# Optimization experiments

Measured on AMD Instinct MI355X. Metric: run time of the kernel, lower is better.

The kernel has to match this reference:

```python
import jax, jax.numpy as jnp
import numpy as np


def setup_inputs() -> dict:
    key = jax.random.key(0)
    kq, kk, kv = jax.random.split(key, 3)
    B, H, S, D = 2, 16, 2048, 64
    Q = jax.random.normal(kq, (B, H, S, D), dtype=jnp.float32)
    K = jax.random.normal(kk, (B, H, S, D), dtype=jnp.float32)
    V = jax.random.normal(kv, (B, H, S, D), dtype=jnp.float32)
    return {"Q": Q, "K": K, "V": V}


def reference(Q, K, V):
    # Faithful to the torch module: NO 1/sqrt(d_k) scaling (d_k is computed
    # but never used in the original forward).
    scores = jnp.einsum('bhqd,bhkd->bhqk', Q, K)      # [B,H,S,S]
    attn = jax.nn.softmax(scores, axis=-1)
    out = jnp.einsum('bhqk,bhkd->bhqd', attn, V)      # [B,H,S,D]
    return out
```

## Files before the change

kernel.cpp:

```cpp
#include <hip/hip_runtime.h>


typedef __bf16 bf16_t;
typedef __bf16 bf16x8 __attribute__((ext_vector_type(8)));
typedef float  f32x16 __attribute__((ext_vector_type(16)));

constexpr int S  = 2048;
constexpr int Dh = 64;
constexpr int QT = 128;
constexpr int KT = 64;

__device__ __forceinline__ int sw(int row, int col) {
    return row * 64 + ((((col >> 3) ^ (row & 7)) << 3) | (col & 7));
}

__global__ __launch_bounds__(256)
void attn_mfma_kernel(const float* __restrict__ Qg,
                      const float* __restrict__ Kg,
                      const float* __restrict__ Vg,
                      float* __restrict__ Og)
{
    __shared__ bf16_t Khs[KT * Dh];
    __shared__ bf16_t Kls[KT * Dh];
    __shared__ bf16_t Vts[Dh * KT];
    __shared__ bf16_t Pbs[QT * Dh];

    const int tid  = threadIdx.x;
    const int lane = tid & 63;
    const int wv   = tid >> 6;
    const int l31  = lane & 31;
    const int l5   = lane >> 5;
    const int mbase = wv * 32;

    const int head = blockIdx.x >> 4;
    const int qt   = blockIdx.x & 15;

    const float* Qp = Qg + ((size_t)head * S + (size_t)qt * QT) * Dh;
    const float* Kp = Kg + (size_t)head * S * Dh;
    const float* Vp = Vg + (size_t)head * S * Dh;
    float*       Op = Og + ((size_t)head * S + (size_t)qt * QT) * Dh;

    bf16x8 qh[4], ql[4];
    {
        const float* qrow = Qp + (size_t)(mbase + l31) * Dh;
        #pragma unroll
        for (int ks = 0; ks < 4; ++ks) {
            const float* p = qrow + ks * 16 + l5 * 8;
            const float4 a = *(const float4*)(p);
            const float4 b = *(const float4*)(p + 4);
            const float xs[8] = {a.x, a.y, a.z, a.w, b.x, b.y, b.z, b.w};
            #pragma unroll
            for (int j = 0; j < 8; ++j) {
                const bf16_t h = (bf16_t)xs[j];
                qh[ks][j] = h;
                ql[ks][j] = (bf16_t)(xs[j] - (float)h);
            }
        }
    }

    f32x16 o0, o1;
    float  lp[16];
    #pragma unroll
    for (int r = 0; r < 16; ++r) { o0[r] = 0.f; o1[r] = 0.f; lp[r] = 0.f; }

    #pragma unroll 1
    for (int ch = 0; ch < S / KT; ++ch) {
        __syncthreads();

        {
            const float* Kc = Kp + (size_t)ch * KT * Dh;
            #pragma unroll
            for (int it = 0; it < 4; ++it) {
                const int f   = it * 256 + tid;
                const int key = f >> 4;
                const int c4  = (f & 15) * 4;
                const float4 kx = *(const float4*)(Kc + key * Dh + c4);
                const float xs[4] = {kx.x, kx.y, kx.z, kx.w};
                union { bf16_t h[4]; uint2 u; } ph, pl;
                #pragma unroll
                for (int j = 0; j < 4; ++j) {
                    const bf16_t h = (bf16_t)xs[j];
                    ph.h[j] = h;
                    pl.h[j] = (bf16_t)(xs[j] - (float)h);
                }
                const int off = sw(key, c4);
                *(uint2*)&Khs[off] = ph.u;
                *(uint2*)&Kls[off] = pl.u;
            }
            const float* Vc = Vp + (size_t)ch * KT * Dh;
            const int kb = (tid >> 4) * 4;
            const int c4 = (tid & 15) * 4;
            const float4 v0 = *(const float4*)(Vc + (size_t)(kb + 0) * Dh + c4);
            const float4 v1 = *(const float4*)(Vc + (size_t)(kb + 1) * Dh + c4);
            const float4 v2 = *(const float4*)(Vc + (size_t)(kb + 2) * Dh + c4);
            const float4 v3 = *(const float4*)(Vc + (size_t)(kb + 3) * Dh + c4);
            const float rs[4][4] = {{v0.x, v1.x, v2.x, v3.x},
                                    {v0.y, v1.y, v2.y, v3.y},
                                    {v0.z, v1.z, v2.z, v3.z},
                                    {v0.w, v1.w, v2.w, v3.w}};
            #pragma unroll
            for (int i = 0; i < 4; ++i) {
                union { bf16_t h[4]; uint2 u; } pv;
                #pragma unroll
                for (int j = 0; j < 4; ++j) pv.h[j] = (bf16_t)rs[i][j];
                *(uint2*)&Vts[sw(c4 + i, kb)] = pv.u;
            }
        }
        __syncthreads();

        f32x16 acc0, acc1;
        #pragma unroll
        for (int r = 0; r < 16; ++r) { acc0[r] = 0.f; acc1[r] = 0.f; }
        #pragma unroll
        for (int ks = 0; ks < 4; ++ks) {
            const int co = ks * 16 + l5 * 8;
            const bf16x8 bh0 = *(const bf16x8*)&Khs[sw(l31,      co)];
            const bf16x8 bh1 = *(const bf16x8*)&Khs[sw(32 + l31, co)];
            const bf16x8 bl0 = *(const bf16x8*)&Kls[sw(l31,      co)];
            const bf16x8 bl1 = *(const bf16x8*)&Kls[sw(32 + l31, co)];
            acc0 = __builtin_amdgcn_mfma_f32_32x32x16_bf16(qh[ks], bh0, acc0, 0, 0, 0);
            acc1 = __builtin_amdgcn_mfma_f32_32x32x16_bf16(qh[ks], bh1, acc1, 0, 0, 0);
            acc0 = __builtin_amdgcn_mfma_f32_32x32x16_bf16(qh[ks], bl0, acc0, 0, 0, 0);
            acc1 = __builtin_amdgcn_mfma_f32_32x32x16_bf16(qh[ks], bl1, acc1, 0, 0, 0);
            acc0 = __builtin_amdgcn_mfma_f32_32x32x16_bf16(ql[ks], bh0, acc0, 0, 0, 0);
            acc1 = __builtin_amdgcn_mfma_f32_32x32x16_bf16(ql[ks], bh1, acc1, 0, 0, 0);
        }

        #pragma unroll
        for (int r = 0; r < 16; ++r) {
            const int row = mbase + (r & 3) + 8 * (r >> 2) + 4 * l5;
            const float p0 = __expf(acc0[r]);
            const float p1 = __expf(acc1[r]);
            const bf16_t b0 = (bf16_t)p0;
            const bf16_t b1 = (bf16_t)p1;
            lp[r] += (float)b0 + (float)b1;
            Pbs[sw(row, l31)]      = b0;
            Pbs[sw(row, 32 + l31)] = b1;
        }

        #pragma unroll
        for (int ks = 0; ks < 4; ++ks) {
            const int co = ks * 16 + l5 * 8;
            const bf16x8 pa  = *(const bf16x8*)&Pbs[sw(mbase + l31, co)];
            const bf16x8 vb0 = *(const bf16x8*)&Vts[sw(l31,      co)];
            const bf16x8 vb1 = *(const bf16x8*)&Vts[sw(32 + l31, co)];
            o0 = __builtin_amdgcn_mfma_f32_32x32x16_bf16(pa, vb0, o0, 0, 0, 0);
            o1 = __builtin_amdgcn_mfma_f32_32x32x16_bf16(pa, vb1, o1, 0, 0, 0);
        }
    }

    #pragma unroll
    for (int r = 0; r < 16; ++r) {
        float v = lp[r];
        #pragma unroll
        for (int m = 1; m <= 16; m <<= 1) v += __shfl_xor(v, m, 64);
        lp[r] = v;
    }

    #pragma unroll
    for (int r = 0; r < 16; ++r) {
        const int row = mbase + (r & 3) + 8 * (r >> 2) + 4 * l5;
        const float inv = 1.0f / lp[r];
        Op[(size_t)row * Dh + l31]      = o0[r] * inv;
        Op[(size_t)row * Dh + 32 + l31] = o1[r] * inv;
    }
}

extern "C" void kernel_launch(void* const* d_in, const int* in_sizes, int n_in,
                              void* d_out, int out_size, void* d_ws, size_t ws_size,
                              hipStream_t stream)
{
    const float* Q = (const float*)d_in[0];
    const float* K = (const float*)d_in[1];
    const float* V = (const float*)d_in[2];
    float*       O = (float*)d_out;

    dim3 grid(32 * (S / QT));
    dim3 block(256);
    attn_mfma_kernel<<<grid, block, 0, stream>>>(Q, K, V, O);
}
```

Before: 169.9 us.

## Split key range across two blocks and combine partial results in second kernel

Each query tile now runs as two blocks that each process half of the key chunks. They write unnormalized partial outputs and row sums to workspace, and a separate combine kernel adds the halves and normalizes. The grid grows from 512 to 1024 blocks so the GPU's CUs are better occupied, and launch bounds now request 4 blocks per SM. The cost is an extra kernel launch plus a round trip of partial outputs through global memory. The split path runs only when the workspace is large enough, otherwise the old path is used.

Result: slower. 439.4 us (+158.6%).

```diff
diff --git a/kernel.cpp b/kernel.cpp
--- a/kernel.cpp
+++ b/kernel.cpp
@@ -14,11 +14,14 @@
     return row * 64 + ((((col >> 3) ^ (row & 7)) << 3) | (col & 7));
 }
 
-__global__ __launch_bounds__(256)
+template<bool SPLIT>
+__global__ __launch_bounds__(256, 4)
 void attn_mfma_kernel(const float* __restrict__ Qg,
                       const float* __restrict__ Kg,
                       const float* __restrict__ Vg,
-                      float* __restrict__ Og)
+                      float* __restrict__ Og,
+                      float* __restrict__ Opart,
+                      float* __restrict__ lpart)
 {
     __shared__ bf16_t Khs[KT * Dh];
     __shared__ bf16_t Kls[KT * Dh];
@@ -32,13 +35,16 @@
     const int l5   = lane >> 5;
     const int mbase = wv * 32;
 
-    const int head = blockIdx.x >> 4;
-    const int qt   = blockIdx.x & 15;
+    const int bx   = blockIdx.x;
+    const int head = SPLIT ? (bx >> 5) : (bx >> 4);
+    const int qt   = SPLIT ? ((bx >> 1) & 15) : (bx & 15);
+    const int half = SPLIT ? (bx & 1) : 0;
+    const int ch0  = SPLIT ? half * (S / KT / 2) : 0;
+    const int nch  = SPLIT ? (S / KT / 2) : (S / KT);
 
     const float* Qp = Qg + ((size_t)head * S + (size_t)qt * QT) * Dh;
     const float* Kp = Kg + (size_t)head * S * Dh;
     const float* Vp = Vg + (size_t)head * S * Dh;
-    float*       Op = Og + ((size_t)head * S + (size_t)qt * QT) * Dh;
 
     bf16x8 qh[4], ql[4];
     {
@@ -64,7 +70,8 @@
     for (int r = 0; r < 16; ++r) { o0[r] = 0.f; o1[r] = 0.f; lp[r] = 0.f; }
 
     #pragma unroll 1
-    for (int ch = 0; ch < S / KT; ++ch) {
+    for (int ci = 0; ci < nch; ++ci) {
+        const int ch = ch0 + ci;
         __syncthreads();
 
         {
@@ -157,13 +164,46 @@
         lp[r] = v;
     }
 
-    #pragma unroll
-    for (int r = 0; r < 16; ++r) {
-        const int row = mbase + (r & 3) + 8 * (r >> 2) + 4 * l5;
-        const float inv = 1.0f / lp[r];
-        Op[(size_t)row * Dh + l31]      = o0[r] * inv;
-        Op[(size_t)row * Dh + 32 + l31] = o1[r] * inv;
-    }
+    if (SPLIT) {
+        float* Po = Opart + (size_t)bx * (QT * Dh);
+        #pragma unroll
+        for (int r = 0; r < 16; ++r) {
+            const int row = mbase + (r & 3) + 8 * (r >> 2) + 4 * l5;
+            Po[(size_t)row * Dh + l31]      = o0[r];
+            Po[(size_t)row * Dh + 32 + l31] = o1[r];
+            if (l31 == 0) lpart[(size_t)bx * QT + row] = lp[r];
+        }
+    } else {
+        float* Op = Og + ((size_t)head * S + (size_t)qt * QT) * Dh;
+        #pragma unroll
+        for (int r = 0; r < 16; ++r) {
+            const int row = mbase + (r & 3) + 8 * (r >> 2) + 4 * l5;
+            const float inv = 1.0f / lp[r];
+            Op[(size_t)row * Dh + l31]      = o0[r] * inv;
+            Op[(size_t)row * Dh + 32 + l31] = o1[r] * inv;
+        }
+    }
+}
+
+__global__ __launch_bounds__(256)
+void combine_kernel(const float* __restrict__ Opart,
+                    const float* __restrict__ lpart,
+                    float* __restrict__ Og)
+{
+    const int i  = blockIdx.x * 256 + threadIdx.x;
+    const int q  = i >> 11;
+    const int rw = (i >> 4) & 127;
+    const size_t e = (size_t)(i & 2047) * 4;
+    const float4 a = *(const float4*)(Opart + (size_t)(2 * q)     * (QT * Dh) + e);
+    const float4 b = *(const float4*)(Opart + (size_t)(2 * q + 1) * (QT * Dh) + e);
+    const float  l = lpart[(size_t)(2 * q) * QT + rw] + lpart[(size_t)(2 * q + 1) * QT + rw];
+    const float inv = 1.0f / l;
+    float4 o;
+    o.x = (a.x + b.x) * inv;
+    o.y = (a.y + b.y) * inv;
+    o.z = (a.z + b.z) * inv;
+    o.w = (a.w + b.w) * inv;
+    *(float4*)(Og + (size_t)i * 4) = o;
 }
 
 extern "C" void kernel_launch(void* const* d_in, const int* in_sizes, int n_in,
@@ -175,7 +215,20 @@
     const float* V = (const float*)d_in[2];
     float*       O = (float*)d_out;
 
-    dim3 grid(32 * (S / QT));
-    dim3 block(256);
-    attn_mfma_kernel<<<grid, block, 0, stream>>>(Q, K, V, O);
-}
+    constexpr size_t NPART       = 1024;
+    constexpr size_t OPART_ELEMS = NPART * QT * Dh;
+    constexpr size_t LPART_ELEMS = NPART * QT;
+    constexpr size_t NEED = (OPART_ELEMS + LPART_ELEMS) * sizeof(float);
+
+    if (ws_size >= NEED) {
+        float* Opart = (float*)d_ws;
+        float* lpart = Opart + OPART_ELEMS;
+        attn_mfma_kernel<true><<<dim3(1024), dim3(256), 0, stream>>>(
+            Q, K, V, nullptr, Opart, lpart);
+        const int n4 = (int)(OPART_ELEMS / 2 / 4);
+        combine_kernel<<<dim3(n4 / 256), dim3(256), 0, stream>>>(Opart, lpart, O);
+    } else {
+        attn_mfma_kernel<false><<<dim3(512), dim3(256), 0, stream>>>(
+            Q, K, V, O, nullptr, nullptr);
+    }
+}
```

## Use single fp16 MFMA for QK^T with 16x16 tiles and 64-row query blocks

Applied to the files above, without the earlier changes.

Replaces the three-pass bf16 hi/lo split for Q·K^T with one fp16 MFMA per tile, which removes the low-part K buffer and roughly two thirds of the score MFMAs. Work moves from 32x32x16 to 16x16x32 MFMA shapes and each block now handles 64 query rows, doubling the grid, with a launch-bounds occupancy hint added. In exchange, every K/V chunk is loaded and converted twice as often across the grid, and fp16 scores carry less mantissa than the split bf16 scheme; softmax still runs without max subtraction.

Measured after the change: 189.5 us. 1.12x slower.

```diff
diff --git a/kernel.cpp b/kernel.cpp
--- a/kernel.cpp
+++ b/kernel.cpp
@@ -1,67 +1,66 @@
 #include <hip/hip_runtime.h>
 
 
-typedef __bf16 bf16_t;
-typedef __bf16 bf16x8 __attribute__((ext_vector_type(8)));
-typedef float  f32x16 __attribute__((ext_vector_type(16)));
+typedef __bf16    bf16_t;
+typedef _Float16  f16_t;
+typedef __bf16    bf16x8 __attribute__((ext_vector_type(8)));
+typedef _Float16  f16x8  __attribute__((ext_vector_type(8)));
+typedef float     f32x4  __attribute__((ext_vector_type(4)));
 
 constexpr int S  = 2048;
 constexpr int Dh = 64;
-constexpr int QT = 128;
 constexpr int KT = 64;
 
 __device__ __forceinline__ int sw(int row, int col) {
     return row * 64 + ((((col >> 3) ^ (row & 7)) << 3) | (col & 7));
 }
 
-__global__ __launch_bounds__(256)
-void attn_mfma_kernel(const float* __restrict__ Qg,
-                      const float* __restrict__ Kg,
-                      const float* __restrict__ Vg,
-                      float* __restrict__ Og)
+__global__ __launch_bounds__(256, 4)
+void attn_kernel(const float* __restrict__ Qg,
+                 const float* __restrict__ Kg,
+                 const float* __restrict__ Vg,
+                 float* __restrict__ Og)
 {
-    __shared__ bf16_t Khs[KT * Dh];
-    __shared__ bf16_t Kls[KT * Dh];
+    __shared__ f16_t  Khs[KT * Dh];
     __shared__ bf16_t Vts[Dh * KT];
-    __shared__ bf16_t Pbs[QT * Dh];
+    __shared__ bf16_t Pbs[64 * KT];
 
     const int tid  = threadIdx.x;
     const int lane = tid & 63;
     const int wv   = tid >> 6;
-    const int l31  = lane & 31;
-    const int l5   = lane >> 5;
-    const int mbase = wv * 32;
+    const int l15  = lane & 15;
+    const int qd   = lane >> 4;
+    const int wb   = wv * 16;
 
-    const int head = blockIdx.x >> 4;
-    const int qt   = blockIdx.x & 15;
+    const int head = blockIdx.x >> 5;
+    const int qt   = blockIdx.x & 31;
 
-    const float* Qp = Qg + ((size_t)head * S + (size_t)qt * QT) * Dh;
+    const float* Qp = Qg + ((size_t)head * S + (size_t)qt * 64) * Dh;
     const float* Kp = Kg + (size_t)head * S * Dh;
     const float* Vp = Vg + (size_t)head * S * Dh;
-    float*       Op = Og + ((size_t)head * S + (size_t)qt * QT) * Dh;
+    float*       Op = Og + ((size_t)head * S + (size_t)qt * 64) * Dh;
 
-    bf16x8 qh[4], ql[4];
+    f16x8 qf[2];
     {
-        const float* qrow = Qp + (size_t)(mbase + l31) * Dh;
+        const float* qrow = Qp + (size_t)(wb + l15) * Dh;
         #pragma unroll
-        for (int ks = 0; ks < 4; ++ks) {
-            const float* p = qrow + ks * 16 + l5 * 8;
+        for (int ks = 0; ks < 2; ++ks) {
+            const float* p = qrow + ks * 32 + qd * 8;
             const float4 a = *(const float4*)(p);
             const float4 b = *(const float4*)(p + 4);
             const float xs[8] = {a.x, a.y, a.z, a.w, b.x, b.y, b.z, b.w};
             #pragma unroll
-            for (int j = 0; j < 8; ++j) {
-                const bf16_t h = (bf16_t)xs[j];
-                qh[ks][j] = h;
-                ql[ks][j] = (bf16_t)(xs[j] - (float)h);
-            }
+            for (int j = 0; j < 8; ++j) qf[ks][j] = (f16_t)xs[j];
         }
     }
 
-    f32x16 o0, o1;
-    float  lp[16];
+    f32x4 oa[4];
+    float lp[4];
     #pragma unroll
-    for (int r = 0; r < 16; ++r) { o0[r] = 0.f; o1[r] = 0.f; lp[r] = 0.f; }
+    for (int t = 0; t < 4; ++t) {
+        oa[t] = (f32x4){0.f, 0.f, 0.f, 0.f};
+        lp[t] = 0.f;
+    }
 
     #pragma unroll 1
     for (int ch = 0; ch < S / KT; ++ch) {
@@ -76,16 +75,10 @@
                 const int c4  = (f & 15) * 4;
                 const float4 kx = *(const float4*)(Kc + key * Dh + c4);
                 const float xs[4] = {kx.x, kx.y, kx.z, kx.w};
-                union { bf16_t h[4]; uint2 u; } ph, pl;
+                union { f16_t h[4]; uint2 u; } ph;
                 #pragma unroll
-                for (int j = 0; j < 4; ++j) {
-                    const bf16_t h = (bf16_t)xs[j];
-                    ph.h[j] = h;
-                    pl.h[j] = (bf16_t)(xs[j] - (float)h);
-                }
-                const int off = sw(key, c4);
-                *(uint2*)&Khs[off] = ph.u;
-                *(uint2*)&Kls[off] = pl.u;
+                for (int j = 0; j < 4; ++j) ph.h[j] = (f16_t)xs[j];
+                *(uint2*)&Khs[sw(key, c4)] = ph.u;
             }
             const float* Vc = Vp + (size_t)ch * KT * Dh;
             const int kb = (tid >> 4) * 4;
@@ -108,61 +101,58 @@
         }
         __syncthreads();
 
-        f32x16 acc0, acc1;
+        f32x4 sc[4];
         #pragma unroll
-        for (int r = 0; r < 16; ++r) { acc0[r] = 0.f; acc1[r] = 0.f; }
+        for (int nt = 0; nt < 4; ++nt) sc[nt] = (f32x4){0.f, 0.f, 0.f, 0.f};
         #pragma unroll
-        for (int ks = 0; ks < 4; ++ks) {
-            const int co = ks * 16 + l5 * 8;
-            const bf16x8 bh0 = *(const bf16x8*)&Khs[sw(l31,      co)];
-            const bf16x8 bh1 = *(const bf16x8*)&Khs[sw(32 + l31, co)];
-            const bf16x8 bl0 = *(const bf16x8*)&Kls[sw(l31,      co)];
-            const bf16x8 bl1 = *(const bf16x8*)&Kls[sw(32 + l31, co)];
-            acc0 = __builtin_amdgcn_mfma_f32_32x32x16_bf16(qh[ks], bh0, acc0, 0, 0, 0);
-            acc1 = __builtin_amdgcn_mfma_f32_32x32x16_bf16(qh[ks], bh1, acc1, 0, 0, 0);
-            acc0 = __builtin_amdgcn_mfma_f32_32x32x16_bf16(qh[ks], bl0, acc0, 0, 0, 0);
-            acc1 = __builtin_amdgcn_mfma_f32_32x32x16_bf16(qh[ks], bl1, acc1, 0, 0, 0);
-            acc0 = __builtin_amdgcn_mfma_f32_32x32x16_bf16(ql[ks], bh0, acc0, 0, 0, 0);
-            acc1 = __builtin_amdgcn_mfma_f32_32x32x16_bf16(ql[ks], bh1, acc1, 0, 0, 0);
+        for (int ks = 0; ks < 2; ++ks) {
+            const int co = ks * 32 + qd * 8;
+            #pragma unroll
+            for (int nt = 0; nt < 4; ++nt) {
+                const f16x8 bk = *(const f16x8*)&Khs[sw(nt * 16 + l15, co)];
+                sc[nt] = __builtin_amdgcn_mfma_f32_16x16x32_f16(qf[ks], bk, sc[nt], 0, 0, 0);
+            }
         }
 
         #pragma unroll
-        for (int r = 0; r < 16; ++r) {
-            const int row = mbase + (r & 3) + 8 * (r >> 2) + 4 * l5;
-            const float p0 = __expf(acc0[r]);
-            const float p1 = __expf(acc1[r]);
-            const bf16_t b0 = (bf16_t)p0;
-            const bf16_t b1 = (bf16_t)p1;
-            lp[r] += (float)b0 + (float)b1;
-            Pbs[sw(row, l31)]      = b0;
-            Pbs[sw(row, 32 + l31)] = b1;
+        for (int nt = 0; nt < 4; ++nt) {
+            #pragma unroll
+            for (int r = 0; r < 4; ++r) {
+                const int row = wb + qd * 4 + r;
+                const bf16_t b = (bf16_t)__expf(sc[nt][r]);
+                lp[r] += (float)b;
+                Pbs[sw(row, nt * 16 + l15)] = b;
+            }
         }
 
         #pragma unroll
-        for (int ks = 0; ks < 4; ++ks) {
-            const int co = ks * 16 + l5 * 8;
-            const bf16x8 pa  = *(const bf16x8*)&Pbs[sw(mbase + l31, co)];
-            const bf16x8 vb0 = *(const bf16x8*)&Vts[sw(l31,      co)];
-            const bf16x8 vb1 = *(const bf16x8*)&Vts[sw(32 + l31, co)];
-            o0 = __builtin_amdgcn_mfma_f32_32x32x16_bf16(pa, vb0, o0, 0, 0, 0);
-            o1 = __builtin_amdgcn_mfma_f32_32x32x16_bf16(pa, vb1, o1, 0, 0, 0);
+        for (int ks = 0; ks < 2; ++ks) {
+            const int co = ks * 32 + qd * 8;
+            const bf16x8 pa = *(const bf16x8*)&Pbs[sw(wb + l15, co)];
+            #pragma unroll
+            for (int dt = 0; dt < 4; ++dt) {
+                const bf16x8 vb = *(const bf16x8*)&Vts[sw(dt * 16 + l15, co)];
+                oa[dt] = __builtin_amdgcn_mfma_f32_16x16x32_bf16(pa, vb, oa[dt], 0, 0, 0);
+            }
         }
     }
 
+    float inv[4];
     #pragma unroll
-    for (int r = 0; r < 16; ++r) {
+    for (int r = 0; r < 4; ++r) {
         float v = lp[r];
         #pragma unroll
-        for (int m = 1; m <= 16; m <<= 1) v += __shfl_xor(v, m, 64);
-        lp[r] = v;
+        for (int m = 1; m <= 8; m <<= 1) v += __shfl_xor(v, m, 64);
+        inv[r] = 1.0f / v;
     }
 
     #pragma unroll
-    for (int r = 0; r < 16; ++r) {
-        const int row = mbase + (r & 3) + 8 * (r >> 2) + 4 * l5;
-        const float inv = 1.0f / lp[r];
-        Op[(size_t)row * Dh + l31]      = o0[r] * inv;
-        Op[(size_t)row * Dh + 32 + l31] = o1[r] * inv;
+    for (int dt = 0; dt < 4; ++dt) {
+        #pragma unroll
+        for (int r = 0; r < 4; ++r) {
+            const int row = wb + qd * 4 + r;
+            Op[(size_t)row * Dh + dt * 16 + l15] = oa[dt][r] * inv[r];
+        }
     }
 }
 
@@ -175,7 +165,7 @@
     const float* V = (const float*)d_in[2];
     float*       O = (float*)d_out;
 
-    dim3 grid(32 * (S / QT));
+    dim3 grid(32 * 32);
     dim3 block(256);
-    attn_mfma_kernel<<<grid, block, 0, stream>>>(Q, K, V, O);
+    attn_kernel<<<grid, block, 0, stream>>>(Q, K, V, O);
 }
```
